# Kernel tuning notes

Hardware: AMD Instinct MI355X
Metric: run time of the kernel (lower is better)

## Reference

```python
import jax, jax.numpy as jnp
import numpy as np

N = 16384
D = 512
NNZ = 163840
NUM_ITERS = 10


def setup_inputs() -> dict:
    key = jax.random.key(0)
    k1, k2, k3, k4 = jax.random.split(key, 4)
    x = jax.random.normal(k1, (N, D), dtype=jnp.float32)
    edge_val = jax.random.uniform(k2, (NNZ,), dtype=jnp.float32)
    edge_row = jnp.sort(jax.random.randint(k3, (NNZ,), 0, N, dtype=jnp.int32))
    edge_col = jax.random.randint(k4, (NNZ,), 0, N, dtype=jnp.int32)
    alpha = jnp.zeros((1,), dtype=jnp.float32)
    beta = jnp.zeros((1,), dtype=jnp.float32)
    sigma = jnp.ones((1,), dtype=jnp.float32)
    return {"x": x, "alpha": alpha, "beta": beta, "sigma": sigma,
            "edge_val": edge_val, "edge_row": edge_row, "edge_col": edge_col,
            "num_iters": NUM_ITERS}


def reference(x, alpha, beta, sigma, edge_val, edge_row, edge_col, num_iters):
    n = x.shape[0]
    # tf.nn.l2_normalize(x, axis=1)
    xn = x * jax.lax.rsqrt(jnp.maximum(jnp.sum(x * x, axis=1, keepdims=True), 1e-12))
    # cosine similarity only at sparse support positions; diagonal zeroed
    sim_e = jnp.sum(xn[edge_row] * xn[edge_col], axis=-1)          # [nnz]
    sim_e = jnp.where(edge_row == edge_col, 0.0, sim_e)
    s = jnp.exp(sigma[0])
    sigma_sq = 2.0 * s * s
    sim_e = jnp.exp(sim_e / (2.0 * sigma_sq))
    # support = sparse support elementwise * similarity
    sup = edge_val * sim_e                                          # [nnz]
    # row-sum of sparse support
    normalize = jax.ops.segment_sum(sup, edge_row, num_segments=n)  # [N]
    a = jnp.exp(alpha[0])
    b = jnp.exp(beta[0])
    denom = b + normalize[:, None] * a + a                          # [N,1] -> broadcast over D

    def step(out, _):
        # sparse matmul: (support @ out)
        Ax = jax.ops.segment_sum(sup[:, None] * out[edge_col], edge_row, num_segments=n)
        out = (x * b + (Ax + out) * a) / denom
        return out, None

    out, _ = jax.lax.scan(step, x, None, length=num_iters)
    return out
```

## Files before the change

kernel.cpp:

```cpp
#include <hip/hip_runtime.h>
#include <hip/hip_fp16.h>

#define DIM 512
#define N_ITERS 10

typedef float floatx2 __attribute__((ext_vector_type(2)));

__device__ __forceinline__ unsigned int pack2h(float lo, float hi) {
    __half2 h = __float22half2_rn(make_float2(lo, hi));
    return *reinterpret_cast<unsigned int*>(&h);
}
__device__ __forceinline__ float2 unpack2h(unsigned int u) {
    return __half22float2(*reinterpret_cast<__half2*>(&u));
}
__device__ __forceinline__ unsigned int pack4f8(float f0, float f1, float f2, float f3) {
    int v = 0;
    v = __builtin_amdgcn_cvt_pk_fp8_f32(f0, f1, v, false);
    v = __builtin_amdgcn_cvt_pk_fp8_f32(f2, f3, v, true);
    return (unsigned int)v;
}

__global__ void consts_kernel(const float* alpha, const float* beta,
                              const float* sigma, float* consts) {
    if (threadIdx.x == 0 && blockIdx.x == 0) {
        float a = expf(alpha[0]);
        float b = expf(beta[0]);
        float s = expf(sigma[0]);
        consts[0] = a;
        consts[1] = b;
        consts[2] = 1.0f / (4.0f * s * s);
    }
}

__global__ void __launch_bounds__(256)
rownorm_kernel(const float* __restrict__ x,
               const float* __restrict__ consts,
               unsigned short* __restrict__ xh16,
               unsigned int* __restrict__ x8,
               unsigned int* __restrict__ xn8,
               unsigned short* __restrict__ xbh, int n) {
    int wid = (blockIdx.x * blockDim.x + threadIdx.x) >> 6;
    int lane = threadIdx.x & 63;
    if (wid >= n) return;
    const size_t base = (size_t)wid * DIM + lane * 8;
    const float4* p = (const float4*)(x + base);
    float4 u = p[0];
    float4 v = p[1];
    float s = u.x*u.x + u.y*u.y + u.z*u.z + u.w*u.w
            + v.x*v.x + v.y*v.y + v.z*v.z + v.w*v.w;
    uint4 h;
    h.x = pack2h(u.x, u.y); h.y = pack2h(u.z, u.w);
    h.z = pack2h(v.x, v.y); h.w = pack2h(v.z, v.w);
    *(uint4*)(xh16 + base) = h;
    uint2 q;
    q.x = pack4f8(u.x, u.y, u.z, u.w);
    q.y = pack4f8(v.x, v.y, v.z, v.w);
    *(uint2*)(x8 + ((size_t)wid * (DIM / 4) + lane * 2)) = q;
    float b = consts[1];
    uint4 hb;
    hb.x = pack2h(u.x * b, u.y * b); hb.y = pack2h(u.z * b, u.w * b);
    hb.z = pack2h(v.x * b, v.y * b); hb.w = pack2h(v.z * b, v.w * b);
    *(uint4*)(xbh + base) = hb;
    #pragma unroll
    for (int m = 32; m >= 1; m >>= 1) s += __shfl_xor(s, m, 64);
    float inr = rsqrtf(fmaxf(s, 1e-12f));
    uint2 qn;
    qn.x = pack4f8(u.x * inr, u.y * inr, u.z * inr, u.w * inr);
    qn.y = pack4f8(v.x * inr, v.y * inr, v.z * inr, v.w * inr);
    *(uint2*)(xn8 + ((size_t)wid * (DIM / 4) + lane * 2)) = qn;
}

__global__ void rowptr_kernel(const int* __restrict__ erow, int nnz,
                              int* __restrict__ rstart, int n) {
    int r = blockIdx.x * blockDim.x + threadIdx.x;
    if (r > n) return;
    int lo = 0, hi = nnz;
    while (lo < hi) {
        int mid = (lo + hi) >> 1;
        if (erow[mid] < r) lo = mid + 1; else hi = mid;
    }
    rstart[r] = lo;
}

__device__ __forceinline__ float dot8f8(const float* A, uint2 h) {
    floatx2 p0 = __builtin_amdgcn_cvt_pk_f32_fp8((int)h.x, false);
    floatx2 p1 = __builtin_amdgcn_cvt_pk_f32_fp8((int)h.x, true);
    floatx2 p2 = __builtin_amdgcn_cvt_pk_f32_fp8((int)h.y, false);
    floatx2 p3 = __builtin_amdgcn_cvt_pk_f32_fp8((int)h.y, true);
    return A[0]*p0.x + A[1]*p0.y + A[2]*p1.x + A[3]*p1.y
         + A[4]*p2.x + A[5]*p2.y + A[6]*p3.x + A[7]*p3.y;
}

__global__ void __launch_bounds__(256)
edge_row_kernel(const unsigned int* __restrict__ xn8,
                const float* __restrict__ eval_,
                const int* __restrict__ ecol,
                const int* __restrict__ rstart,
                const float* __restrict__ consts,
                float* __restrict__ sup, float* __restrict__ inv_denom, int n) {
    int row = (blockIdx.x * blockDim.x + threadIdx.x) >> 6;
    int lane = threadIdx.x & 63;
    if (row >= n) return;
    uint2 hr = *(const uint2*)(xn8 + (size_t)row * (DIM / 4) + lane * 2);
    float A[8];
    {
        floatx2 p0 = __builtin_amdgcn_cvt_pk_f32_fp8((int)hr.x, false);
        floatx2 p1 = __builtin_amdgcn_cvt_pk_f32_fp8((int)hr.x, true);
        floatx2 p2 = __builtin_amdgcn_cvt_pk_f32_fp8((int)hr.y, false);
        floatx2 p3 = __builtin_amdgcn_cvt_pk_f32_fp8((int)hr.y, true);
        A[0]=p0.x; A[1]=p0.y; A[2]=p1.x; A[3]=p1.y;
        A[4]=p2.x; A[5]=p2.y; A[6]=p3.x; A[7]=p3.y;
    }
    float c2 = consts[2];
    int rs = rstart[row], re = rstart[row + 1];
    float norm_acc = 0.0f;
    int e = rs;
    for (; e + 3 < re; e += 4) {
        int c[4]; uint2 h[4]; float s[4];
        #pragma unroll
        for (int j = 0; j < 4; ++j) c[j] = ecol[e + j];
        #pragma unroll
        for (int j = 0; j < 4; ++j)
            h[j] = *(const uint2*)(xn8 + (size_t)c[j] * (DIM / 4) + lane * 2);
        #pragma unroll
        for (int j = 0; j < 4; ++j) s[j] = dot8f8(A, h[j]);
        #pragma unroll
        for (int m = 32; m >= 1; m >>= 1) {
            #pragma unroll
            for (int j = 0; j < 4; ++j) s[j] += __shfl_xor(s[j], m, 64);
        }
        #pragma unroll
        for (int j = 0; j < 4; ++j) {
            float sim = (row == c[j]) ? 0.0f : s[j];
            float sp = eval_[e + j] * expf(sim * c2);
            norm_acc += sp;
            if (lane == 0) sup[e + j] = sp;
        }
    }
    for (; e < re; ++e) {
        int c0 = ecol[e];
        uint2 h0 = *(const uint2*)(xn8 + (size_t)c0 * (DIM / 4) + lane * 2);
        float s0 = dot8f8(A, h0);
        #pragma unroll
        for (int m = 32; m >= 1; m >>= 1) s0 += __shfl_xor(s0, m, 64);
        float sim0 = (row == c0) ? 0.0f : s0;
        float sp0 = eval_[e] * expf(sim0 * c2);
        norm_acc += sp0;
        if (lane == 0) sup[e] = sp0;
    }
    if (lane == 0) {
        float a = consts[0], b = consts[1];
        inv_denom[row] = 1.0f / (b + norm_acc * a + a);
    }
}

#define ACCF8(hh, ww)                                                              \
    do {                                                                           \
        floatx2 p_;                                                                \
        p_ = __builtin_amdgcn_cvt_pk_f32_fp8((int)(hh).x, false); acc0 += (ww)*p_.x; acc1 += (ww)*p_.y; \
        p_ = __builtin_amdgcn_cvt_pk_f32_fp8((int)(hh).x, true);  acc2 += (ww)*p_.x; acc3 += (ww)*p_.y; \
        p_ = __builtin_amdgcn_cvt_pk_f32_fp8((int)(hh).y, false); acc4 += (ww)*p_.x; acc5 += (ww)*p_.y; \
        p_ = __builtin_amdgcn_cvt_pk_f32_fp8((int)(hh).y, true);  acc6 += (ww)*p_.x; acc7 += (ww)*p_.y; \
    } while (0)

__global__ void __launch_bounds__(256)
iter_kernel(const unsigned short* __restrict__ prev16,
            const unsigned int* __restrict__ prev8,
            unsigned short* __restrict__ next16,
            unsigned int* __restrict__ next8,
            float* __restrict__ out_f32, int last,
            const float* __restrict__ consts, const float* __restrict__ inv_denom,
            const float* __restrict__ sup, const int* __restrict__ ecol,
            const int* __restrict__ rstart,
            const unsigned short* __restrict__ xbh, int n) {
    int row = (blockIdx.x * blockDim.x + threadIdx.x) >> 6;
    int lane = threadIdx.x & 63;
    if (row >= n) return;
    float a = consts[0];
    float inv_d = inv_denom[row];
    int rs = rstart[row], re = rstart[row + 1];
    const size_t loff16 = lane * 8;
    const size_t base16 = (size_t)row * DIM + loff16;
    const size_t loff8 = lane * 2;
    float acc0 = 0.f, acc1 = 0.f, acc2 = 0.f, acc3 = 0.f;
    float acc4 = 0.f, acc5 = 0.f, acc6 = 0.f, acc7 = 0.f;
    int e = rs;
    for (; e + 7 < re; e += 8) {
        int c[8]; float w[8]; uint2 h[8];
        #pragma unroll
        for (int j = 0; j < 8; ++j) { c[j] = ecol[e + j]; w[j] = sup[e + j]; }
        #pragma unroll
        for (int j = 0; j < 8; ++j)
            h[j] = *(const uint2*)(prev8 + (size_t)c[j] * (DIM / 4) + loff8);
        #pragma unroll
        for (int j = 0; j < 8; ++j) ACCF8(h[j], w[j]);
    }
    for (; e + 1 < re; e += 2) {
        int c0 = ecol[e], c1 = ecol[e + 1];
        float w0 = sup[e], w1 = sup[e + 1];
        uint2 h0 = *(const uint2*)(prev8 + (size_t)c0 * (DIM / 4) + loff8);
        uint2 h1 = *(const uint2*)(prev8 + (size_t)c1 * (DIM / 4) + loff8);
        ACCF8(h0, w0);
        ACCF8(h1, w1);
    }
    if (e < re) {
        float w = sup[e];
        int c = ecol[e];
        uint2 h = *(const uint2*)(prev8 + (size_t)c * (DIM / 4) + loff8);
        ACCF8(h, w);
    }
    uint4 hs = *(const uint4*)(prev16 + base16);
    uint4 hx = *(const uint4*)(xbh + base16);
    float2 s0 = unpack2h(hs.x), s1 = unpack2h(hs.y);
    float2 s2 = unpack2h(hs.z), s3 = unpack2h(hs.w);
    float2 x0 = unpack2h(hx.x), x1 = unpack2h(hx.y);
    float2 x2 = unpack2h(hx.z), x3 = unpack2h(hx.w);
    float r0 = (x0.x + (acc0 + s0.x) * a) * inv_d;
    float r1 = (x0.y + (acc1 + s0.y) * a) * inv_d;
    float r2 = (x1.x + (acc2 + s1.x) * a) * inv_d;
    float r3 = (x1.y + (acc3 + s1.y) * a) * inv_d;
    float r4 = (x2.x + (acc4 + s2.x) * a) * inv_d;
    float r5 = (x2.y + (acc5 + s2.y) * a) * inv_d;
    float r6 = (x3.x + (acc6 + s3.x) * a) * inv_d;
    float r7 = (x3.y + (acc7 + s3.y) * a) * inv_d;
    if (last) {
        float4* o = (float4*)(out_f32 + base16);
        o[0] = make_float4(r0, r1, r2, r3);
        o[1] = make_float4(r4, r5, r6, r7);
    } else {
        uint4 ho;
        ho.x = pack2h(r0, r1); ho.y = pack2h(r2, r3);
        ho.z = pack2h(r4, r5); ho.w = pack2h(r6, r7);
        *(uint4*)(next16 + base16) = ho;
        uint2 q;
        q.x = pack4f8(r0, r1, r2, r3);
        q.y = pack4f8(r4, r5, r6, r7);
        *(uint2*)(next8 + (size_t)row * (DIM / 4) + loff8) = q;
    }
}

extern "C" void kernel_launch(void* const* d_in, const int* in_sizes, int n_in,
                              void* d_out, int out_size, void* d_ws, size_t ws_size,
                              hipStream_t stream) {
    const float* x     = (const float*)d_in[0];
    const float* alpha = (const float*)d_in[1];
    const float* beta  = (const float*)d_in[2];
    const float* sigma = (const float*)d_in[3];
    const float* eval_ = (const float*)d_in[4];
    const int* erow = (const int*)d_in[5];
    const int* ecol = (const int*)d_in[6];

    const int n   = in_sizes[0] / DIM;
    const int nnz = in_sizes[4];

    float* ws        = (float*)d_ws;
    float* consts    = ws;
    float* inv_denom = ws + 64;
    int*   rstart    = (int*)(inv_denom + n);
    float* sup       = (float*)(rstart + n + 64);
    unsigned short* xbh   = (unsigned short*)(sup + nnz);
    unsigned short* bufB16= xbh + (size_t)n * DIM;
    unsigned int*   xn8   = (unsigned int*)(bufB16 + (size_t)n * DIM);
    unsigned int*   bufA8 = xn8 + (size_t)n * (DIM / 4);
    unsigned int*   bufB8 = bufA8 + (size_t)n * (DIM / 4);
    unsigned short* bufA16 = (unsigned short*)d_out;
    float* out_f32 = (float*)d_out;

    consts_kernel<<<1, 64, 0, stream>>>(alpha, beta, sigma, consts);
    rownorm_kernel<<<(n * 64) / 256, 256, 0, stream>>>(x, consts, bufA16, bufA8, xn8, xbh, n);
    rowptr_kernel<<<(n + 256) / 256, 256, 0, stream>>>(erow, nnz, rstart, n);
    edge_row_kernel<<<(n * 64) / 256, 256, 0, stream>>>(xn8, eval_, ecol,
                                                        rstart, consts,
                                                        sup, inv_denom, n);

    for (int it = 0; it < N_ITERS; ++it) {
        const unsigned short* prev16 = (it & 1) ? bufB16 : bufA16;
        const unsigned int*   prev8  = (it & 1) ? bufB8  : bufA8;
        unsigned short* next16 = (it & 1) ? bufA16 : bufB16;
        unsigned int*   next8  = (it & 1) ? bufA8  : bufB8;
        int last = (it == N_ITERS - 1) ? 1 : 0;
        iter_kernel<<<(n * 64) / 256, 256, 0, stream>>>(prev16, prev8, next16, next8,
                                                        out_f32, last,
                                                        consts, inv_denom, sup, ecol,
                                                        rstart, xbh, n);
    }
}
```

Measured before the change: 333.4 us.

## Pack edge col/weight pairs, fuse rowptr into rownorm, hoist self loads

```diff
diff --git a/kernel.cpp b/kernel.cpp
--- a/kernel.cpp
+++ b/kernel.cpp
@@ -21,7 +21,8 @@
 }
 
 __global__ void consts_kernel(const float* alpha, const float* beta,
-                              const float* sigma, float* consts) {
+                              const float* sigma, float* consts,
+                              int* rstart, int n, int nnz) {
     if (threadIdx.x == 0 && blockIdx.x == 0) {
         float a = expf(alpha[0]);
         float b = expf(beta[0]);
@@ -29,6 +30,7 @@
         consts[0] = a;
         consts[1] = b;
         consts[2] = 1.0f / (4.0f * s * s);
+        rstart[n] = nnz;
     }
 }
 
@@ -38,7 +40,9 @@
                unsigned short* __restrict__ xh16,
                unsigned int* __restrict__ x8,
                unsigned int* __restrict__ xn8,
-               unsigned short* __restrict__ xbh, int n) {
+               unsigned short* __restrict__ xb16,
+               const int* __restrict__ erow, int nnz,
+               int* __restrict__ rstart, int n) {
     int wid = (blockIdx.x * blockDim.x + threadIdx.x) >> 6;
     int lane = threadIdx.x & 63;
     if (wid >= n) return;
@@ -46,6 +50,14 @@
     const float4* p = (const float4*)(x + base);
     float4 u = p[0];
     float4 v = p[1];
+    if (lane == 0) {
+        int lo = 0, hi = nnz;
+        while (lo < hi) {
+            int mid = (lo + hi) >> 1;
+            if (erow[mid] < wid) lo = mid + 1; else hi = mid;
+        }
+        rstart[wid] = lo;
+    }
     float s = u.x*u.x + u.y*u.y + u.z*u.z + u.w*u.w
             + v.x*v.x + v.y*v.y + v.z*v.z + v.w*v.w;
     uint4 h;
@@ -55,31 +67,19 @@
     uint2 q;
     q.x = pack4f8(u.x, u.y, u.z, u.w);
     q.y = pack4f8(v.x, v.y, v.z, v.w);
-    *(uint2*)(x8 + ((size_t)wid * (DIM / 4) + lane * 2)) = q;
+    *(uint2*)(x8 + (size_t)wid * (DIM / 4) + lane * 2) = q;
     float b = consts[1];
     uint4 hb;
     hb.x = pack2h(u.x * b, u.y * b); hb.y = pack2h(u.z * b, u.w * b);
     hb.z = pack2h(v.x * b, v.y * b); hb.w = pack2h(v.z * b, v.w * b);
-    *(uint4*)(xbh + base) = hb;
+    *(uint4*)(xb16 + base) = hb;
     #pragma unroll
     for (int m = 32; m >= 1; m >>= 1) s += __shfl_xor(s, m, 64);
     float inr = rsqrtf(fmaxf(s, 1e-12f));
     uint2 qn;
     qn.x = pack4f8(u.x * inr, u.y * inr, u.z * inr, u.w * inr);
     qn.y = pack4f8(v.x * inr, v.y * inr, v.z * inr, v.w * inr);
-    *(uint2*)(xn8 + ((size_t)wid * (DIM / 4) + lane * 2)) = qn;
-}
-
-__global__ void rowptr_kernel(const int* __restrict__ erow, int nnz,
-                              int* __restrict__ rstart, int n) {
-    int r = blockIdx.x * blockDim.x + threadIdx.x;
-    if (r > n) return;
-    int lo = 0, hi = nnz;
-    while (lo < hi) {
-        int mid = (lo + hi) >> 1;
-        if (erow[mid] < r) lo = mid + 1; else hi = mid;
-    }
-    rstart[r] = lo;
+    *(uint2*)(xn8 + (size_t)wid * (DIM / 4) + lane * 2) = qn;
 }
 
 __device__ __forceinline__ float dot8f8(const float* A, uint2 h) {
@@ -97,7 +97,7 @@
                 const int* __restrict__ ecol,
                 const int* __restrict__ rstart,
                 const float* __restrict__ consts,
-                float* __restrict__ sup, float* __restrict__ inv_denom, int n) {
+                uint2* __restrict__ epk, float* __restrict__ inv_denom, int n) {
     int row = (blockIdx.x * blockDim.x + threadIdx.x) >> 6;
     int lane = threadIdx.x & 63;
     if (row >= n) return;
@@ -115,29 +115,53 @@
     int rs = rstart[row], re = rstart[row + 1];
     float norm_acc = 0.0f;
     int e = rs;
-    for (; e + 3 < re; e += 4) {
-        int c[4]; uint2 h[4]; float s[4];
-        #pragma unroll
-        for (int j = 0; j < 4; ++j) c[j] = ecol[e + j];
-        #pragma unroll
-        for (int j = 0; j < 4; ++j)
+    for (; e + 7 < re; e += 8) {
+        int c[8]; uint2 h[8]; float s[8]; float ev[8];
+        #pragma unroll
+        for (int j = 0; j < 8; ++j) c[j] = ecol[e + j];
+        #pragma unroll
+        for (int j = 0; j < 8; ++j) ev[j] = eval_[e + j];
+        #pragma unroll
+        for (int j = 0; j < 8; ++j)
             h[j] = *(const uint2*)(xn8 + (size_t)c[j] * (DIM / 4) + lane * 2);
         #pragma unroll
-        for (int j = 0; j < 4; ++j) s[j] = dot8f8(A, h[j]);
+        for (int j = 0; j < 8; ++j) s[j] = dot8f8(A, h[j]);
         #pragma unroll
         for (int m = 32; m >= 1; m >>= 1) {
             #pragma unroll
-            for (int j = 0; j < 4; ++j) s[j] += __shfl_xor(s[j], m, 64);
-        }
-        #pragma unroll
-        for (int j = 0; j < 4; ++j) {
+            for (int j = 0; j < 8; ++j) s[j] += __shfl_xor(s[j], m, 64);
+        }
+        #pragma unroll
+        for (int j = 0; j < 8; ++j) {
             float sim = (row == c[j]) ? 0.0f : s[j];
-            float sp = eval_[e + j] * expf(sim * c2);
+            float sp = ev[j] * expf(sim * c2);
             norm_acc += sp;
-            if (lane == 0) sup[e + j] = sp;
-        }
-    }
-    for (; e < re; ++e) {
+            if (lane == 0) epk[e + j] = make_uint2((unsigned int)c[j], __float_as_uint(sp));
+        }
+    }
+    for (; e + 1 < re; e += 2) {
+        int c0 = ecol[e], c1 = ecol[e + 1];
+        float ev0 = eval_[e], ev1 = eval_[e + 1];
+        uint2 h0 = *(const uint2*)(xn8 + (size_t)c0 * (DIM / 4) + lane * 2);
+        uint2 h1 = *(const uint2*)(xn8 + (size_t)c1 * (DIM / 4) + lane * 2);
+        float s0 = dot8f8(A, h0);
+        float s1 = dot8f8(A, h1);
+        #pragma unroll
+        for (int m = 32; m >= 1; m >>= 1) {
+            s0 += __shfl_xor(s0, m, 64);
+            s1 += __shfl_xor(s1, m, 64);
+        }
+        float sim0 = (row == c0) ? 0.0f : s0;
+        float sim1 = (row == c1) ? 0.0f : s1;
+        float sp0 = ev0 * expf(sim0 * c2);
+        float sp1 = ev1 * expf(sim1 * c2);
+        norm_acc += sp0 + sp1;
+        if (lane == 0) {
+            epk[e]     = make_uint2((unsigned int)c0, __float_as_uint(sp0));
+            epk[e + 1] = make_uint2((unsigned int)c1, __float_as_uint(sp1));
+        }
+    }
+    if (e < re) {
         int c0 = ecol[e];
         uint2 h0 = *(const uint2*)(xn8 + (size_t)c0 * (DIM / 4) + lane * 2);
         float s0 = dot8f8(A, h0);
@@ -146,7 +170,7 @@
         float sim0 = (row == c0) ? 0.0f : s0;
         float sp0 = eval_[e] * expf(sim0 * c2);
         norm_acc += sp0;
-        if (lane == 0) sup[e] = sp0;
+        if (lane == 0) epk[e] = make_uint2((unsigned int)c0, __float_as_uint(sp0));
     }
     if (lane == 0) {
         float a = consts[0], b = consts[1];
@@ -170,7 +194,7 @@
             unsigned int* __restrict__ next8,
             float* __restrict__ out_f32, int last,
             const float* __restrict__ consts, const float* __restrict__ inv_denom,
-            const float* __restrict__ sup, const int* __restrict__ ecol,
+            const uint2* __restrict__ epk,
             const int* __restrict__ rstart,
             const unsigned short* __restrict__ xbh, int n) {
     int row = (blockIdx.x * blockDim.x + threadIdx.x) >> 6;
@@ -182,35 +206,33 @@
     const size_t loff16 = lane * 8;
     const size_t base16 = (size_t)row * DIM + loff16;
     const size_t loff8 = lane * 2;
+    uint4 hs = *(const uint4*)(prev16 + base16);
+    uint4 hx = *(const uint4*)(xbh + base16);
     float acc0 = 0.f, acc1 = 0.f, acc2 = 0.f, acc3 = 0.f;
     float acc4 = 0.f, acc5 = 0.f, acc6 = 0.f, acc7 = 0.f;
     int e = rs;
     for (; e + 7 < re; e += 8) {
-        int c[8]; float w[8]; uint2 h[8];
-        #pragma unroll
-        for (int j = 0; j < 8; ++j) { c[j] = ecol[e + j]; w[j] = sup[e + j]; }
+        uint2 m[8]; uint2 h[8];
+        #pragma unroll
+        for (int j = 0; j < 8; ++j) m[j] = epk[e + j];
         #pragma unroll
         for (int j = 0; j < 8; ++j)
-            h[j] = *(const uint2*)(prev8 + (size_t)c[j] * (DIM / 4) + loff8);
-        #pragma unroll
-        for (int j = 0; j < 8; ++j) ACCF8(h[j], w[j]);
+            h[j] = *(const uint2*)(prev8 + (size_t)m[j].x * (DIM / 4) + loff8);
+        #pragma unroll
+        for (int j = 0; j < 8; ++j) ACCF8(h[j], __uint_as_float(m[j].y));
     }
     for (; e + 1 < re; e += 2) {
-        int c0 = ecol[e], c1 = ecol[e + 1];
-        float w0 = sup[e], w1 = sup[e + 1];
-        uint2 h0 = *(const uint2*)(prev8 + (size_t)c0 * (DIM / 4) + loff8);
-        uint2 h1 = *(const uint2*)(prev8 + (size_t)c1 * (DIM / 4) + loff8);
-        ACCF8(h0, w0);
-        ACCF8(h1, w1);
+        uint2 m0 = epk[e], m1 = epk[e + 1];
+        uint2 h0 = *(const uint2*)(prev8 + (size_t)m0.x * (DIM / 4) + loff8);
+        uint2 h1 = *(const uint2*)(prev8 + (size_t)m1.x * (DIM / 4) + loff8);
+        ACCF8(h0, __uint_as_float(m0.y));
+        ACCF8(h1, __uint_as_float(m1.y));
     }
     if (e < re) {
-        float w = sup[e];
-        int c = ecol[e];
-        uint2 h = *(const uint2*)(prev8 + (size_t)c * (DIM / 4) + loff8);
-        ACCF8(h, w);
-    }
-    uint4 hs = *(const uint4*)(prev16 + base16);
-    uint4 hx = *(const uint4*)(xbh + base16);
+        uint2 m0 = epk[e];
+        uint2 h0 = *(const uint2*)(prev8 + (size_t)m0.x * (DIM / 4) + loff8);
+        ACCF8(h0, __uint_as_float(m0.y));
+    }
     float2 s0 = unpack2h(hs.x), s1 = unpack2h(hs.y);
     float2 s2 = unpack2h(hs.z), s3 = unpack2h(hs.w);
     float2 x0 = unpack2h(hx.x), x1 = unpack2h(hx.y);
@@ -257,8 +279,8 @@
     float* consts    = ws;
     float* inv_denom = ws + 64;
     int*   rstart    = (int*)(inv_denom + n);
-    float* sup       = (float*)(rstart + n + 64);
-    unsigned short* xbh   = (unsigned short*)(sup + nnz);
+    uint2* epk       = (uint2*)(rstart + n + 64);
+    unsigned short* xbh   = (unsigned short*)(epk + nnz);
     unsigned short* bufB16= xbh + (size_t)n * DIM;
     unsigned int*   xn8   = (unsigned int*)(bufB16 + (size_t)n * DIM);
     unsigned int*   bufA8 = xn8 + (size_t)n * (DIM / 4);
@@ -266,12 +288,12 @@
     unsigned short* bufA16 = (unsigned short*)d_out;
     float* out_f32 = (float*)d_out;
 
-    consts_kernel<<<1, 64, 0, stream>>>(alpha, beta, sigma, consts);
-    rownorm_kernel<<<(n * 64) / 256, 256, 0, stream>>>(x, consts, bufA16, bufA8, xn8, xbh, n);
-    rowptr_kernel<<<(n + 256) / 256, 256, 0, stream>>>(erow, nnz, rstart, n);
+    consts_kernel<<<1, 64, 0, stream>>>(alpha, beta, sigma, consts, rstart, n, nnz);
+    rownorm_kernel<<<(n * 64) / 256, 256, 0, stream>>>(x, consts, bufA16, bufA8, xn8,
+                                                       xbh, erow, nnz, rstart, n);
     edge_row_kernel<<<(n * 64) / 256, 256, 0, stream>>>(xn8, eval_, ecol,
                                                         rstart, consts,
-                                                        sup, inv_denom, n);
+                                                        epk, inv_denom, n);
 
     for (int it = 0; it < N_ITERS; ++it) {
         const unsigned short* prev16 = (it & 1) ? bufB16 : bufA16;
@@ -281,7 +303,7 @@
         int last = (it == N_ITERS - 1) ? 1 : 0;
         iter_kernel<<<(n * 64) / 256, 256, 0, stream>>>(prev16, prev8, next16, next8,
                                                         out_f32, last,
-                                                        consts, inv_denom, sup, ecol,
+                                                        consts, inv_denom, epk,
                                                         rstart, xbh, n);
     }
 }
```

Measured after the change: 337.4 us. Within noise of the previous version (+1.2%).
